# Kernel tuning notes

Measured on AMD Instinct MI355X. Metric: run time of the kernel, lower is better.

## Reference

```python
import jax, jax.numpy as jnp
import numpy as np

B, S, H = 2, 2048, 2048
N_HEADS = 16
HEAD_DIM = H // N_HEADS


def setup_inputs() -> dict:
    key = jax.random.key(0)
    ks = jax.random.split(key, 9)
    s = 1.0 / np.sqrt(H)
    inp = {
        "x": jax.random.normal(ks[0], (B, S, H), dtype=jnp.float32),
        "wq": jax.random.uniform(ks[1], (H, H), jnp.float32, -s, s),
        "bq": jnp.zeros((H,), jnp.float32),
        "wk": jax.random.uniform(ks[2], (H, H), jnp.float32, -s, s),
        "bk": jnp.zeros((H,), jnp.float32),
        "wv": jax.random.uniform(ks[3], (H, H), jnp.float32, -s, s),
        "bv": jnp.zeros((H,), jnp.float32),
        "wo": jax.random.uniform(ks[4], (H, H), jnp.float32, -s, s),
        "bo": jnp.zeros((H,), jnp.float32),
    }
    return inp


def reference(x, wq, bq, wk, bk, wv, bv, wo, bo):
    bsz, seq_len, hidden = x.shape
    scale = HEAD_DIM ** -0.5
    # projections -> [b, h, s, d]
    def proj(w, b):
        y = jnp.einsum("bsh,oh->bso", x, w) + b
        return y.reshape(bsz, seq_len, N_HEADS, HEAD_DIM).transpose(0, 2, 1, 3)
    q = proj(wq, bq)
    k = proj(wk, bk)
    v = proj(wv, bv)
    scores = jnp.einsum("bhqd,bhkd->bhqk", q, k) * scale
    causal = jnp.tril(jnp.ones((seq_len, seq_len), dtype=bool))
    scores = jnp.where(causal, scores, -jnp.inf)
    attn = jax.nn.softmax(scores, axis=-1)
    out = jnp.einsum("bhqk,bhkd->bhqd", attn, v)
    out = out.transpose(0, 2, 1, 3).reshape(bsz, seq_len, hidden)
    return jnp.einsum("bsh,oh->bso", out, wo) + bo
```

## Files before the change

### kernel.cpp

```cpp
#include <hip/hip_runtime.h>
#include <hip/hip_bf16.h>
#include <cstdint>
#include <cstddef>

#define BATCH 2
#define S_LEN 2048
#define HID   2048
#define NH    16
#define HD    128
#define ATT_TILES (32 * NH * BATCH)

typedef short bf16x8 __attribute__((ext_vector_type(8)));
typedef float f32x4  __attribute__((ext_vector_type(4)));

__device__ inline unsigned short f2bf(float f) {
    unsigned int u = __float_as_uint(f);
    unsigned int r = (u + 0x7fffu + ((u >> 16) & 1u)) >> 16;
    return (unsigned short)r;
}

__global__ __launch_bounds__(256) void conv_f32_bf16(const float* __restrict__ src,
                                                     unsigned short* __restrict__ dst,
                                                     long n) {
    long i = ((long)blockIdx.x * 256 + threadIdx.x) * 8;
    if (i >= n) return;
    const float4 a = *(const float4*)(src + i);
    const float4 b = *(const float4*)(src + i + 4);
    union { unsigned short u[8]; bf16x8 v; } o;
    o.u[0] = f2bf(a.x); o.u[1] = f2bf(a.y); o.u[2] = f2bf(a.z); o.u[3] = f2bf(a.w);
    o.u[4] = f2bf(b.x); o.u[5] = f2bf(b.y); o.u[6] = f2bf(b.z); o.u[7] = f2bf(b.w);
    *(bf16x8*)(dst + i) = o.v;
}

__global__ __launch_bounds__(256) void conv4_f32_bf16(const float* __restrict__ s0,
                                                      const float* __restrict__ s1,
                                                      const float* __restrict__ s2,
                                                      const float* __restrict__ s3,
                                                      unsigned short* __restrict__ d0,
                                                      unsigned short* __restrict__ d1,
                                                      unsigned short* __restrict__ d2,
                                                      unsigned short* __restrict__ d3,
                                                      long n) {
    const int z = blockIdx.y;
    const float* src = (z == 0) ? s0 : (z == 1) ? s1 : (z == 2) ? s2 : s3;
    unsigned short* dst = (z == 0) ? d0 : (z == 1) ? d1 : (z == 2) ? d2 : d3;
    long i = ((long)blockIdx.x * 256 + threadIdx.x) * 8;
    if (i >= n) return;
    const float4 a = *(const float4*)(src + i);
    const float4 b = *(const float4*)(src + i + 4);
    union { unsigned short u[8]; bf16x8 v; } o;
    o.u[0] = f2bf(a.x); o.u[1] = f2bf(a.y); o.u[2] = f2bf(a.z); o.u[3] = f2bf(a.w);
    o.u[4] = f2bf(b.x); o.u[5] = f2bf(b.y); o.u[6] = f2bf(b.z); o.u[7] = f2bf(b.w);
    *(bf16x8*)(dst + i) = o.v;
}

__global__ void zero_int(int* p) { *p = 0; }

__device__ __forceinline__ void gemm_core(const unsigned short* __restrict__ A,
                                          const unsigned short* __restrict__ Bw,
                                          const float* __restrict__ bias,
                                          void* __restrict__ Cout,
                                          int M, int N, int K, int mode,
                                          int m0, int n0,
                                          unsigned short* Sm) {
    unsigned short* As = Sm;
    unsigned short* Bs = Sm + 4096;
    const int tid = threadIdx.x;
    const int lane = tid & 63;
    const int wave = tid >> 6;
    const int g = lane >> 4, ln = lane & 15;
    const int wm = (wave & 1) * 64, wn = (wave >> 1) * 64;

    f32x4 acc[4][4];
#pragma unroll
    for (int i = 0; i < 4; ++i)
#pragma unroll
        for (int j = 0; j < 4; ++j) acc[i][j] = (f32x4){0.f, 0.f, 0.f, 0.f};

    const int srow = wave * 16 + (lane >> 2);
    const int scol = (((lane & 3) ^ ((lane >> 3) & 3)) * 8);
    const int rxor = (ln >> 1) & 3;

    for (int k0 = 0; k0 < K; k0 += 32) {
#pragma unroll
        for (int c = 0; c < 2; ++c) {
            const unsigned short* ga = A  + (size_t)(m0 + c * 64 + srow) * K + k0 + scol;
            const unsigned short* gb = Bw + (size_t)(n0 + c * 64 + srow) * K + k0 + scol;
            __builtin_amdgcn_global_load_lds(
                (const __attribute__((address_space(1))) void*)ga,
                (__attribute__((address_space(3))) void*)(As + c * 2048 + wave * 512),
                16, 0, 0);
            __builtin_amdgcn_global_load_lds(
                (const __attribute__((address_space(1))) void*)gb,
                (__attribute__((address_space(3))) void*)(Bs + c * 2048 + wave * 512),
                16, 0, 0);
        }
        __syncthreads();
        bf16x8 af[4], bfr[4];
#pragma unroll
        for (int t = 0; t < 4; ++t) {
            af[t]  = *(const bf16x8*)&As[(wm + t * 16 + ln) * 32 + (g ^ rxor) * 8];
            bfr[t] = *(const bf16x8*)&Bs[(wn + t * 16 + ln) * 32 + (g ^ rxor) * 8];
        }
#pragma unroll
        for (int mt = 0; mt < 4; ++mt)
#pragma unroll
            for (int nt = 0; nt < 4; ++nt)
                acc[mt][nt] = __builtin_amdgcn_mfma_f32_16x16x32_bf16(af[mt], bfr[nt], acc[mt][nt], 0, 0, 0);
        __syncthreads();
    }

    if (mode == 1) {
        const int b = m0 >> 11;
        const int sbase = m0 & 2047;
        const int h = n0 >> 7;
#pragma unroll
        for (int p2 = 0; p2 < 2; ++p2) {
            if ((wave >> 1) == p2) {
#pragma unroll
                for (int nt = 0; nt < 4; ++nt) {
                    const int dl = nt * 16 + ln;
                    const float bn = bias[n0 + p2 * 64 + dl];
#pragma unroll
                    for (int mt = 0; mt < 4; ++mt)
#pragma unroll
                        for (int r = 0; r < 4; ++r) {
                            const int sl = wm + mt * 16 + g * 4 + r;
                            const int psc = (sl >> 3) ^ (dl & 15);
                            Sm[dl * 128 + psc * 8 + (sl & 7)] = f2bf(acc[mt][nt][r] + bn);
                        }
                }
            }
            __syncthreads();
            const int dl = tid >> 2;
            const int dd = p2 * 64 + dl;
            unsigned short* dst = (unsigned short*)Cout +
                ((size_t)(b * NH + h) * HD + dd) * S_LEN + sbase;
#pragma unroll
            for (int j = 0; j < 4; ++j) {
                const int sc = (tid & 3) * 4 + j;
                const int psc = sc ^ (dl & 15);
                *(bf16x8*)(dst + sc * 8) = *(const bf16x8*)&Sm[dl * 128 + psc * 8];
            }
            __syncthreads();
        }
        return;
    }

#pragma unroll
    for (int mt = 0; mt < 4; ++mt)
#pragma unroll
        for (int nt = 0; nt < 4; ++nt) {
            const int n = n0 + wn + nt * 16 + ln;
            const float bn = bias[n];
#pragma unroll
            for (int r = 0; r < 4; ++r) {
                const int m = m0 + wm + mt * 16 + g * 4 + r;
                const float v = acc[mt][nt][r] + bn;
                if (mode == 2) {
                    ((float*)Cout)[(size_t)m * N + n] = v;
                } else {
                    const int b = m >> 11, s = m & 2047;
                    const int h = n >> 7, d = n & 127;
                    ((unsigned short*)Cout)[((((size_t)b * NH + h) * S_LEN + s) * HD + d)] = f2bf(v);
                }
            }
        }
}

__global__ __launch_bounds__(256) void gemm_qkv(const unsigned short* __restrict__ A,
                                                const unsigned short* __restrict__ w0,
                                                const unsigned short* __restrict__ w1,
                                                const unsigned short* __restrict__ w2,
                                                const float* __restrict__ b0,
                                                const float* __restrict__ b1,
                                                const float* __restrict__ b2,
                                                void* o0, void* o1, void* o2,
                                                int M, int N, int K) {
    __shared__ __align__(16) unsigned short Sm[8192];
    const int z = blockIdx.z;
    const unsigned short* Bw = (z == 0) ? w0 : (z == 1) ? w1 : w2;
    const float* bias = (z == 0) ? b0 : (z == 1) ? b1 : b2;
    void* Cout = (z == 0) ? o0 : (z == 1) ? o1 : o2;
    const int mode = (z == 2) ? 1 : 0;
    gemm_core(A, Bw, bias, Cout, M, N, K, mode,
              blockIdx.y * 128, blockIdx.x * 128, Sm);
}

__global__ __launch_bounds__(256) void gemm_bt(const unsigned short* __restrict__ A,
                                               const unsigned short* __restrict__ Bw,
                                               const float* __restrict__ bias,
                                               void* __restrict__ Cout,
                                               int M, int N, int K, int mode) {
    __shared__ __align__(16) unsigned short Sm[8192];
    gemm_core(A, Bw, bias, Cout, M, N, K, mode,
              blockIdx.y * 128, blockIdx.x * 128, Sm);
}

__global__ __launch_bounds__(256) void attn_kernel(const unsigned short* __restrict__ Q,
                                                   const unsigned short* __restrict__ Kk,
                                                   const unsigned short* __restrict__ Vt,
                                                   unsigned short* __restrict__ O,
                                                   int* __restrict__ ticket) {
    __shared__ __align__(16) unsigned short Ks[64 * 128];
    __shared__ __align__(16) unsigned short Vs[144 * 64];
    __shared__ __align__(16) unsigned short Pl[4][16 * 72];
    __shared__ int tsh;
    const int tid = threadIdx.x;
    const int lane = tid & 63;
    const int wave = tid >> 6;
    const int g = lane >> 4, ln = lane & 15;
    const float scale2 = 0.08838834764831845f * 1.4426950408889634f;

    for (int i = tid; i < 16 * 64; i += 256) Vs[128 * 64 + i] = 0x3F80;

    const int kcol = ((tid & 15) ^ ((tid >> 4) & 15)) * 8;
    const int vcol = ((tid & 7) ^ ((tid >> 3) & 7)) * 8;

    for (;;) {
        if (tid == 0) tsh = atomicAdd(ticket, 1);
        __syncthreads();
        const int t = tsh;
        if (t >= ATT_TILES) break;
        const int qt = 31 - (t >> 5);
        const int bh = t & 31;
        const int qbase = qt * 64 + wave * 16;

        const unsigned short* Qp = Q  + (size_t)bh * S_LEN * HD;
        const unsigned short* Kp = Kk + (size_t)bh * S_LEN * HD;
        const unsigned short* Vp = Vt + (size_t)bh * HD * S_LEN;

        bf16x8 aq[4];
#pragma unroll
        for (int dc = 0; dc < 4; ++dc)
            aq[dc] = *(const bf16x8*)&Qp[(size_t)(qbase + ln) * HD + dc * 32 + g * 8];

        f32x4 acc[9];
#pragma unroll
        for (int i = 0; i < 9; ++i) acc[i] = (f32x4){0.f, 0.f, 0.f, 0.f};

        for (int kt = 0; kt <= qt; ++kt) {
            const int kb = kt * 64;
#pragma unroll
            for (int i = 0; i < 4; ++i) {
                const unsigned short* gk = Kp + (size_t)(kb + i * 16 + (tid >> 4)) * HD + kcol;
                __builtin_amdgcn_global_load_lds(
                    (const __attribute__((address_space(1))) void*)gk,
                    (__attribute__((address_space(3))) void*)(Ks + i * 2048 + wave * 512),
                    16, 0, 0);
            }
#pragma unroll
            for (int i = 0; i < 4; ++i) {
                const unsigned short* gv = Vp + (size_t)(i * 32 + (tid >> 3)) * S_LEN + kb + vcol;
                __builtin_amdgcn_global_load_lds(
                    (const __attribute__((address_space(1))) void*)gv,
                    (__attribute__((address_space(3))) void*)(Vs + i * 2048 + wave * 512),
                    16, 0, 0);
            }
            __syncthreads();
            f32x4 sc[4];
#pragma unroll
            for (int nc = 0; nc < 4; ++nc) {
                sc[nc] = (f32x4){0.f, 0.f, 0.f, 0.f};
#pragma unroll
                for (int dc = 0; dc < 4; ++dc) {
                    bf16x8 bk = *(const bf16x8*)&Ks[(nc * 16 + ln) * 128 + ((dc * 4 + g) ^ ln) * 8];
                    sc[nc] = __builtin_amdgcn_mfma_f32_16x16x32_bf16(aq[dc], bk, sc[nc], 0, 0, 0);
                }
            }
            const bool diag = (kt == qt);
#pragma unroll
            for (int nc = 0; nc < 4; ++nc)
#pragma unroll
                for (int r = 0; r < 4; ++r) {
                    float pv = __builtin_amdgcn_exp2f(sc[nc][r] * scale2);
                    if (diag && (nc * 16 + ln > wave * 16 + g * 4 + r)) pv = 0.f;
                    Pl[wave][(g * 4 + r) * 72 + nc * 16 + ln] = f2bf(pv);
                }
#pragma unroll
            for (int kc = 0; kc < 2; ++kc) {
                bf16x8 ap = *(const bf16x8*)&Pl[wave][ln * 72 + kc * 32 + g * 8];
#pragma unroll
                for (int d2 = 0; d2 < 9; ++d2) {
                    bf16x8 bv = *(const bf16x8*)&Vs[(d2 * 16 + ln) * 64 + ((kc * 4 + g) ^ (ln & 7)) * 8];
                    acc[d2] = __builtin_amdgcn_mfma_f32_16x16x32_bf16(ap, bv, acc[d2], 0, 0, 0);
                }
            }
            __syncthreads();
        }
        const int b = bh >> 4, h = bh & 15;
        float inv[4];
#pragma unroll
        for (int r = 0; r < 4; ++r) inv[r] = 1.0f / acc[8][r];
#pragma unroll
        for (int d2 = 0; d2 < 8; ++d2)
#pragma unroll
            for (int r = 0; r < 4; ++r) {
                const int row = qbase + g * 4 + r;
                const int col = h * HD + d2 * 16 + ln;
                O[((size_t)b * S_LEN + row) * HID + col] = f2bf(acc[d2][r] * inv[r]);
            }
    }
}

extern "C" void kernel_launch(void* const* d_in, const int* in_sizes, int n_in,
                              void* d_out, int out_size, void* d_ws, size_t ws_size,
                              hipStream_t stream) {
    const float* x  = (const float*)d_in[0];
    const float* wq = (const float*)d_in[1];
    const float* bq = (const float*)d_in[2];
    const float* wk = (const float*)d_in[3];
    const float* bk = (const float*)d_in[4];
    const float* wv = (const float*)d_in[5];
    const float* bv = (const float*)d_in[6];
    const float* wo = (const float*)d_in[7];
    const float* bo = (const float*)d_in[8];
    float* out = (float*)d_out;

    const long nx = (long)BATCH * S_LEN * HID;
    const long nw = (long)HID * HID;

    char* p = (char*)d_ws;
    unsigned short* xb  = (unsigned short*)p; p += nx * 2;
    unsigned short* wqb = (unsigned short*)p; p += nw * 2;
    unsigned short* wkb = (unsigned short*)p; p += nw * 2;
    unsigned short* wvb = (unsigned short*)p; p += nw * 2;
    unsigned short* wob = (unsigned short*)p; p += nw * 2;
    unsigned short* Qb  = (unsigned short*)p; p += nx * 2;
    unsigned short* Kb  = (unsigned short*)p; p += nx * 2;
    unsigned short* Vtb = (unsigned short*)p; p += nx * 2;
    unsigned short* Ob  = (unsigned short*)p; p += nx * 2;
    int* ticket = (int*)p;

    conv_f32_bf16<<<(int)(nx / 8 / 256), 256, 0, stream>>>(x, xb, nx);
    dim3 cgrid((unsigned)(nw / 8 / 256), 4);
    conv4_f32_bf16<<<cgrid, 256, 0, stream>>>(wq, wk, wv, wo, wqb, wkb, wvb, wob, nw);
    zero_int<<<1, 1, 0, stream>>>(ticket);

    const int M = BATCH * S_LEN;
    dim3 qkvgrid(HID / 128, M / 128, 3);
    gemm_qkv<<<qkvgrid, 256, 0, stream>>>(xb, wqb, wkb, wvb, bq, bk, bv,
                                          Qb, Kb, Vtb, M, HID, HID);

    attn_kernel<<<768, 256, 0, stream>>>(Qb, Kb, Vtb, Ob, ticket);

    dim3 ggrid(HID / 128, M / 128);
    gemm_bt<<<ggrid, 256, 0, stream>>>(Ob, wob, bo, out, M, HID, HID, 2);
}
```

Before: 433.5 us.

## Use 128-row attention tiles with 8 waves and split-K output GEMM with atomics

```diff
diff --git a/kernel.cpp b/kernel.cpp
--- a/kernel.cpp
+++ b/kernel.cpp
@@ -8,7 +8,7 @@
 #define HID   2048
 #define NH    16
 #define HD    128
-#define ATT_TILES (32 * NH * BATCH)
+#define ATT_TILES2 (16 * NH * BATCH)
 
 typedef short bf16x8 __attribute__((ext_vector_type(8)));
 typedef float f32x4  __attribute__((ext_vector_type(4)));
@@ -56,12 +56,17 @@
 
 __global__ void zero_int(int* p) { *p = 0; }
 
+__global__ __launch_bounds__(256) void zero_f32(float4* __restrict__ p, long n4) {
+    long i = (long)blockIdx.x * 256 + threadIdx.x;
+    if (i < n4) p[i] = (float4){0.f, 0.f, 0.f, 0.f};
+}
+
 __device__ __forceinline__ void gemm_core(const unsigned short* __restrict__ A,
                                           const unsigned short* __restrict__ Bw,
                                           const float* __restrict__ bias,
                                           void* __restrict__ Cout,
                                           int M, int N, int K, int mode,
-                                          int m0, int n0,
+                                          int m0, int n0, int kbeg, int kend,
                                           unsigned short* Sm) {
     unsigned short* As = Sm;
     unsigned short* Bs = Sm + 4096;
@@ -81,7 +86,7 @@
     const int scol = (((lane & 3) ^ ((lane >> 3) & 3)) * 8);
     const int rxor = (ln >> 1) & 3;
 
-    for (int k0 = 0; k0 < K; k0 += 32) {
+    for (int k0 = kbeg; k0 < kend; k0 += 32) {
 #pragma unroll
         for (int c = 0; c < 2; ++c) {
             const unsigned short* ga = A  + (size_t)(m0 + c * 64 + srow) * K + k0 + scol;
@@ -152,13 +157,13 @@
 #pragma unroll
         for (int nt = 0; nt < 4; ++nt) {
             const int n = n0 + wn + nt * 16 + ln;
-            const float bn = bias[n];
+            const float bn = (mode != 3 || kbeg == 0) ? bias[n] : 0.f;
 #pragma unroll
             for (int r = 0; r < 4; ++r) {
                 const int m = m0 + wm + mt * 16 + g * 4 + r;
                 const float v = acc[mt][nt][r] + bn;
-                if (mode == 2) {
-                    ((float*)Cout)[(size_t)m * N + n] = v;
+                if (mode == 3) {
+                    atomicAdd(&((float*)Cout)[(size_t)m * N + n], v);
                 } else {
                     const int b = m >> 11, s = m & 2047;
                     const int h = n >> 7, d = n & 127;
@@ -184,27 +189,29 @@
     void* Cout = (z == 0) ? o0 : (z == 1) ? o1 : o2;
     const int mode = (z == 2) ? 1 : 0;
     gemm_core(A, Bw, bias, Cout, M, N, K, mode,
-              blockIdx.y * 128, blockIdx.x * 128, Sm);
-}
-
-__global__ __launch_bounds__(256) void gemm_bt(const unsigned short* __restrict__ A,
-                                               const unsigned short* __restrict__ Bw,
-                                               const float* __restrict__ bias,
-                                               void* __restrict__ Cout,
-                                               int M, int N, int K, int mode) {
+              blockIdx.y * 128, blockIdx.x * 128, 0, K, Sm);
+}
+
+__global__ __launch_bounds__(256) void gemm_out(const unsigned short* __restrict__ A,
+                                                const unsigned short* __restrict__ Bw,
+                                                const float* __restrict__ bias,
+                                                void* __restrict__ Cout,
+                                                int M, int N, int K) {
     __shared__ __align__(16) unsigned short Sm[8192];
-    gemm_core(A, Bw, bias, Cout, M, N, K, mode,
-              blockIdx.y * 128, blockIdx.x * 128, Sm);
-}
-
-__global__ __launch_bounds__(256) void attn_kernel(const unsigned short* __restrict__ Q,
+    const int kh = K / 2;
+    gemm_core(A, Bw, bias, Cout, M, N, K, 3,
+              blockIdx.y * 128, blockIdx.x * 128,
+              blockIdx.z * kh, blockIdx.z * kh + kh, Sm);
+}
+
+__global__ __launch_bounds__(512) void attn_kernel(const unsigned short* __restrict__ Q,
                                                    const unsigned short* __restrict__ Kk,
                                                    const unsigned short* __restrict__ Vt,
                                                    unsigned short* __restrict__ O,
                                                    int* __restrict__ ticket) {
     __shared__ __align__(16) unsigned short Ks[64 * 128];
     __shared__ __align__(16) unsigned short Vs[144 * 64];
-    __shared__ __align__(16) unsigned short Pl[4][16 * 72];
+    __shared__ __align__(16) unsigned short Pl[8][16 * 72];
     __shared__ int tsh;
     const int tid = threadIdx.x;
     const int lane = tid & 63;
@@ -212,7 +219,7 @@
     const int g = lane >> 4, ln = lane & 15;
     const float scale2 = 0.08838834764831845f * 1.4426950408889634f;
 
-    for (int i = tid; i < 16 * 64; i += 256) Vs[128 * 64 + i] = 0x3F80;
+    for (int i = tid; i < 16 * 64; i += 512) Vs[128 * 64 + i] = 0x3F80;
 
     const int kcol = ((tid & 15) ^ ((tid >> 4) & 15)) * 8;
     const int vcol = ((tid & 7) ^ ((tid >> 3) & 7)) * 8;
@@ -221,10 +228,10 @@
         if (tid == 0) tsh = atomicAdd(ticket, 1);
         __syncthreads();
         const int t = tsh;
-        if (t >= ATT_TILES) break;
-        const int qt = 31 - (t >> 5);
+        if (t >= ATT_TILES2) break;
+        const int qt = 15 - (t >> 5);
         const int bh = t & 31;
-        const int qbase = qt * 64 + wave * 16;
+        const int qbase = qt * 128 + wave * 16;
 
         const unsigned short* Qp = Q  + (size_t)bh * S_LEN * HD;
         const unsigned short* Kp = Kk + (size_t)bh * S_LEN * HD;
@@ -239,51 +246,56 @@
 #pragma unroll
         for (int i = 0; i < 9; ++i) acc[i] = (f32x4){0.f, 0.f, 0.f, 0.f};
 
-        for (int kt = 0; kt <= qt; ++kt) {
+        const int ktend = 2 * qt + 1;
+        const int myktmax = 2 * qt + (wave >> 2);
+        for (int kt = 0; kt <= ktend; ++kt) {
             const int kb = kt * 64;
 #pragma unroll
-            for (int i = 0; i < 4; ++i) {
-                const unsigned short* gk = Kp + (size_t)(kb + i * 16 + (tid >> 4)) * HD + kcol;
+            for (int i = 0; i < 2; ++i) {
+                const unsigned short* gk = Kp + (size_t)(kb + i * 32 + (tid >> 4)) * HD + kcol;
                 __builtin_amdgcn_global_load_lds(
                     (const __attribute__((address_space(1))) void*)gk,
-                    (__attribute__((address_space(3))) void*)(Ks + i * 2048 + wave * 512),
+                    (__attribute__((address_space(3))) void*)(Ks + i * 4096 + wave * 512),
                     16, 0, 0);
             }
 #pragma unroll
-            for (int i = 0; i < 4; ++i) {
-                const unsigned short* gv = Vp + (size_t)(i * 32 + (tid >> 3)) * S_LEN + kb + vcol;
+            for (int i = 0; i < 2; ++i) {
+                const unsigned short* gv = Vp + (size_t)(i * 64 + (tid >> 3)) * S_LEN + kb + vcol;
                 __builtin_amdgcn_global_load_lds(
                     (const __attribute__((address_space(1))) void*)gv,
-                    (__attribute__((address_space(3))) void*)(Vs + i * 2048 + wave * 512),
+                    (__attribute__((address_space(3))) void*)(Vs + i * 4096 + wave * 512),
                     16, 0, 0);
             }
             __syncthreads();
-            f32x4 sc[4];
-#pragma unroll
-            for (int nc = 0; nc < 4; ++nc) {
-                sc[nc] = (f32x4){0.f, 0.f, 0.f, 0.f};
-#pragma unroll
-                for (int dc = 0; dc < 4; ++dc) {
-                    bf16x8 bk = *(const bf16x8*)&Ks[(nc * 16 + ln) * 128 + ((dc * 4 + g) ^ ln) * 8];
-                    sc[nc] = __builtin_amdgcn_mfma_f32_16x16x32_bf16(aq[dc], bk, sc[nc], 0, 0, 0);
+            if (kt <= myktmax) {
+                f32x4 sc[4];
+#pragma unroll
+                for (int nc = 0; nc < 4; ++nc) {
+                    sc[nc] = (f32x4){0.f, 0.f, 0.f, 0.f};
+#pragma unroll
+                    for (int dc = 0; dc < 4; ++dc) {
+                        bf16x8 bk = *(const bf16x8*)&Ks[(nc * 16 + ln) * 128 + ((dc * 4 + g) ^ ln) * 8];
+                        sc[nc] = __builtin_amdgcn_mfma_f32_16x16x32_bf16(aq[dc], bk, sc[nc], 0, 0, 0);
+                    }
                 }
-            }
-            const bool diag = (kt == qt);
-#pragma unroll
-            for (int nc = 0; nc < 4; ++nc)
-#pragma unroll
-                for (int r = 0; r < 4; ++r) {
-                    float pv = __builtin_amdgcn_exp2f(sc[nc][r] * scale2);
-                    if (diag && (nc * 16 + ln > wave * 16 + g * 4 + r)) pv = 0.f;
-                    Pl[wave][(g * 4 + r) * 72 + nc * 16 + ln] = f2bf(pv);
-                }
-#pragma unroll
-            for (int kc = 0; kc < 2; ++kc) {
-                bf16x8 ap = *(const bf16x8*)&Pl[wave][ln * 72 + kc * 32 + g * 8];
-#pragma unroll
-                for (int d2 = 0; d2 < 9; ++d2) {
-                    bf16x8 bv = *(const bf16x8*)&Vs[(d2 * 16 + ln) * 64 + ((kc * 4 + g) ^ (ln & 7)) * 8];
-                    acc[d2] = __builtin_amdgcn_mfma_f32_16x16x32_bf16(ap, bv, acc[d2], 0, 0, 0);
+                const bool diag = (kt == myktmax);
+                const int lrow = (wave & 3) * 16;
+#pragma unroll
+                for (int nc = 0; nc < 4; ++nc)
+#pragma unroll
+                    for (int r = 0; r < 4; ++r) {
+                        float pv = __builtin_amdgcn_exp2f(sc[nc][r] * scale2);
+                        if (diag && (nc * 16 + ln > lrow + g * 4 + r)) pv = 0.f;
+                        Pl[wave][(g * 4 + r) * 72 + nc * 16 + ln] = f2bf(pv);
+                    }
+#pragma unroll
+                for (int kc = 0; kc < 2; ++kc) {
+                    bf16x8 ap = *(const bf16x8*)&Pl[wave][ln * 72 + kc * 32 + g * 8];
+#pragma unroll
+                    for (int d2 = 0; d2 < 9; ++d2) {
+                        bf16x8 bv = *(const bf16x8*)&Vs[(d2 * 16 + ln) * 64 + ((kc * 4 + g) ^ (ln & 7)) * 8];
+                        acc[d2] = __builtin_amdgcn_mfma_f32_16x16x32_bf16(ap, bv, acc[d2], 0, 0, 0);
+                    }
                 }
             }
             __syncthreads();
@@ -336,14 +348,15 @@
     dim3 cgrid((unsigned)(nw / 8 / 256), 4);
     conv4_f32_bf16<<<cgrid, 256, 0, stream>>>(wq, wk, wv, wo, wqb, wkb, wvb, wob, nw);
     zero_int<<<1, 1, 0, stream>>>(ticket);
+    zero_f32<<<(int)(nx / 4 / 256), 256, 0, stream>>>((float4*)out, nx / 4);
 
     const int M = BATCH * S_LEN;
     dim3 qkvgrid(HID / 128, M / 128, 3);
     gemm_qkv<<<qkvgrid, 256, 0, stream>>>(xb, wqb, wkb, wvb, bq, bk, bv,
                                           Qb, Kb, Vtb, M, HID, HID);
 
-    attn_kernel<<<768, 256, 0, stream>>>(Qb, Kb, Vtb, Ob, ticket);
-
-    dim3 ggrid(HID / 128, M / 128);
-    gemm_bt<<<ggrid, 256, 0, stream>>>(Ob, wob, bo, out, M, HID, HID, 2);
-}
+    attn_kernel<<<512, 512, 0, stream>>>(Qb, Kb, Vtb, Ob, ticket);
+
+    dim3 ogrid(HID / 128, M / 128, 2);
+    gemm_out<<<ogrid, 256, 0, stream>>>(Ob, wob, bo, out, M, HID, HID);
+}
```

Result: slower. 466.4 us (+7.6%).

## Fuse Q and K projections into one GEMM sharing the activation tile

Applied to the files above, without the earlier changes.

```diff
diff --git a/kernel.cpp b/kernel.cpp
--- a/kernel.cpp
+++ b/kernel.cpp
@@ -56,19 +56,108 @@
 
 __global__ void zero_int(int* p) { *p = 0; }
 
-__device__ __forceinline__ void gemm_core(const unsigned short* __restrict__ A,
-                                          const unsigned short* __restrict__ Bw,
-                                          const float* __restrict__ bias,
-                                          void* __restrict__ Cout,
-                                          int M, int N, int K, int mode,
-                                          int m0, int n0,
-                                          unsigned short* Sm) {
+__global__ __launch_bounds__(256) void gemm_qk(const unsigned short* __restrict__ A,
+                                               const unsigned short* __restrict__ wqb,
+                                               const unsigned short* __restrict__ wkb,
+                                               const float* __restrict__ bq,
+                                               const float* __restrict__ bk,
+                                               unsigned short* __restrict__ Qo,
+                                               unsigned short* __restrict__ Ko,
+                                               int M, int N, int K) {
+    __shared__ __align__(16) unsigned short As [128 * 32];
+    __shared__ __align__(16) unsigned short Bsq[128 * 32];
+    __shared__ __align__(16) unsigned short Bsk[128 * 32];
+    const int tid = threadIdx.x;
+    const int lane = tid & 63;
+    const int wave = tid >> 6;
+    const int g = lane >> 4, ln = lane & 15;
+    const int m0 = blockIdx.y * 128, n0 = blockIdx.x * 128;
+    const int wm = (wave & 1) * 64, wn = (wave >> 1) * 64;
+
+    f32x4 accq[4][4], acck[4][4];
+#pragma unroll
+    for (int i = 0; i < 4; ++i)
+#pragma unroll
+        for (int j = 0; j < 4; ++j) {
+            accq[i][j] = (f32x4){0.f, 0.f, 0.f, 0.f};
+            acck[i][j] = (f32x4){0.f, 0.f, 0.f, 0.f};
+        }
+
+    const int srow = wave * 16 + (lane >> 2);
+    const int scol = (((lane & 3) ^ ((lane >> 3) & 3)) * 8);
+    const int rxor = (ln >> 1) & 3;
+
+    for (int k0 = 0; k0 < K; k0 += 32) {
+#pragma unroll
+        for (int c = 0; c < 2; ++c) {
+            const size_t roff = (size_t)(c * 64 + srow) * K + k0 + scol;
+            __builtin_amdgcn_global_load_lds(
+                (const __attribute__((address_space(1))) void*)(A + (size_t)m0 * K + roff),
+                (__attribute__((address_space(3))) void*)(As + c * 2048 + wave * 512), 16, 0, 0);
+            __builtin_amdgcn_global_load_lds(
+                (const __attribute__((address_space(1))) void*)(wqb + (size_t)n0 * K + roff),
+                (__attribute__((address_space(3))) void*)(Bsq + c * 2048 + wave * 512), 16, 0, 0);
+            __builtin_amdgcn_global_load_lds(
+                (const __attribute__((address_space(1))) void*)(wkb + (size_t)n0 * K + roff),
+                (__attribute__((address_space(3))) void*)(Bsk + c * 2048 + wave * 512), 16, 0, 0);
+        }
+        __syncthreads();
+        bf16x8 af[4], bfr[4];
+#pragma unroll
+        for (int t = 0; t < 4; ++t)
+            af[t] = *(const bf16x8*)&As[(wm + t * 16 + ln) * 32 + (g ^ rxor) * 8];
+#pragma unroll
+        for (int t = 0; t < 4; ++t)
+            bfr[t] = *(const bf16x8*)&Bsq[(wn + t * 16 + ln) * 32 + (g ^ rxor) * 8];
+#pragma unroll
+        for (int mt = 0; mt < 4; ++mt)
+#pragma unroll
+            for (int nt = 0; nt < 4; ++nt)
+                accq[mt][nt] = __builtin_amdgcn_mfma_f32_16x16x32_bf16(af[mt], bfr[nt], accq[mt][nt], 0, 0, 0);
+#pragma unroll
+        for (int t = 0; t < 4; ++t)
+            bfr[t] = *(const bf16x8*)&Bsk[(wn + t * 16 + ln) * 32 + (g ^ rxor) * 8];
+#pragma unroll
+        for (int mt = 0; mt < 4; ++mt)
+#pragma unroll
+            for (int nt = 0; nt < 4; ++nt)
+                acck[mt][nt] = __builtin_amdgcn_mfma_f32_16x16x32_bf16(af[mt], bfr[nt], acck[mt][nt], 0, 0, 0);
+        __syncthreads();
+    }
+
+    const int bb = m0 >> 11;
+    const int sbase = m0 & 2047;
+    const int hh = n0 >> 7;
+#pragma unroll
+    for (int mt = 0; mt < 4; ++mt)
+#pragma unroll
+        for (int nt = 0; nt < 4; ++nt) {
+            const int n = wn + nt * 16 + ln;
+            const float bnq = bq[n0 + n];
+            const float bnk = bk[n0 + n];
+#pragma unroll
+            for (int r = 0; r < 4; ++r) {
+                const int s = sbase + wm + mt * 16 + g * 4 + r;
+                const size_t idx = (((size_t)(bb * NH + hh) * S_LEN + s) * HD + n);
+                Qo[idx] = f2bf(accq[mt][nt][r] + bnq);
+                Ko[idx] = f2bf(acck[mt][nt][r] + bnk);
+            }
+        }
+}
+
+__global__ __launch_bounds__(256) void gemm_v(const unsigned short* __restrict__ A,
+                                              const unsigned short* __restrict__ Bw,
+                                              const float* __restrict__ bias,
+                                              unsigned short* __restrict__ Vo,
+                                              int M, int N, int K) {
+    __shared__ __align__(16) unsigned short Sm[8192];
     unsigned short* As = Sm;
     unsigned short* Bs = Sm + 4096;
     const int tid = threadIdx.x;
     const int lane = tid & 63;
     const int wave = tid >> 6;
     const int g = lane >> 4, ln = lane & 15;
+    const int m0 = blockIdx.y * 128, n0 = blockIdx.x * 128;
     const int wm = (wave & 1) * 64, wn = (wave >> 1) * 64;
 
     f32x4 acc[4][4];
@@ -88,12 +177,10 @@
             const unsigned short* gb = Bw + (size_t)(n0 + c * 64 + srow) * K + k0 + scol;
             __builtin_amdgcn_global_load_lds(
                 (const __attribute__((address_space(1))) void*)ga,
-                (__attribute__((address_space(3))) void*)(As + c * 2048 + wave * 512),
-                16, 0, 0);
+                (__attribute__((address_space(3))) void*)(As + c * 2048 + wave * 512), 16, 0, 0);
             __builtin_amdgcn_global_load_lds(
                 (const __attribute__((address_space(1))) void*)gb,
-                (__attribute__((address_space(3))) void*)(Bs + c * 2048 + wave * 512),
-                16, 0, 0);
+                (__attribute__((address_space(3))) void*)(Bs + c * 2048 + wave * 512), 16, 0, 0);
         }
         __syncthreads();
         bf16x8 af[4], bfr[4];
@@ -110,41 +197,89 @@
         __syncthreads();
     }
 
-    if (mode == 1) {
-        const int b = m0 >> 11;
-        const int sbase = m0 & 2047;
-        const int h = n0 >> 7;
-#pragma unroll
-        for (int p2 = 0; p2 < 2; ++p2) {
-            if ((wave >> 1) == p2) {
-#pragma unroll
-                for (int nt = 0; nt < 4; ++nt) {
-                    const int dl = nt * 16 + ln;
-                    const float bn = bias[n0 + p2 * 64 + dl];
-#pragma unroll
-                    for (int mt = 0; mt < 4; ++mt)
-#pragma unroll
-                        for (int r = 0; r < 4; ++r) {
-                            const int sl = wm + mt * 16 + g * 4 + r;
-                            const int psc = (sl >> 3) ^ (dl & 15);
-                            Sm[dl * 128 + psc * 8 + (sl & 7)] = f2bf(acc[mt][nt][r] + bn);
-                        }
-                }
-            }
-            __syncthreads();
-            const int dl = tid >> 2;
-            const int dd = p2 * 64 + dl;
-            unsigned short* dst = (unsigned short*)Cout +
-                ((size_t)(b * NH + h) * HD + dd) * S_LEN + sbase;
-#pragma unroll
-            for (int j = 0; j < 4; ++j) {
-                const int sc = (tid & 3) * 4 + j;
-                const int psc = sc ^ (dl & 15);
-                *(bf16x8*)(dst + sc * 8) = *(const bf16x8*)&Sm[dl * 128 + psc * 8];
-            }
-            __syncthreads();
-        }
-        return;
+    const int b = m0 >> 11;
+    const int sbase = m0 & 2047;
+    const int h = n0 >> 7;
+#pragma unroll
+    for (int p2 = 0; p2 < 2; ++p2) {
+        if ((wave >> 1) == p2) {
+#pragma unroll
+            for (int nt = 0; nt < 4; ++nt) {
+                const int dl = nt * 16 + ln;
+                const float bn = bias[n0 + p2 * 64 + dl];
+#pragma unroll
+                for (int mt = 0; mt < 4; ++mt)
+#pragma unroll
+                    for (int r = 0; r < 4; ++r) {
+                        const int sl = wm + mt * 16 + g * 4 + r;
+                        const int psc = (sl >> 3) ^ (dl & 15);
+                        Sm[dl * 128 + psc * 8 + (sl & 7)] = f2bf(acc[mt][nt][r] + bn);
+                    }
+            }
+        }
+        __syncthreads();
+        const int dl = tid >> 2;
+        const int dd = p2 * 64 + dl;
+        unsigned short* dst = Vo + ((size_t)(b * NH + h) * HD + dd) * S_LEN + sbase;
+#pragma unroll
+        for (int j = 0; j < 4; ++j) {
+            const int sc = (tid & 3) * 4 + j;
+            const int psc = sc ^ (dl & 15);
+            *(bf16x8*)(dst + sc * 8) = *(const bf16x8*)&Sm[dl * 128 + psc * 8];
+        }
+        __syncthreads();
+    }
+}
+
+__global__ __launch_bounds__(256) void gemm_bt(const unsigned short* __restrict__ A,
+                                               const unsigned short* __restrict__ Bw,
+                                               const float* __restrict__ bias,
+                                               float* __restrict__ Cout,
+                                               int M, int N, int K) {
+    __shared__ __align__(16) unsigned short As[128 * 32];
+    __shared__ __align__(16) unsigned short Bs[128 * 32];
+    const int tid = threadIdx.x;
+    const int lane = tid & 63;
+    const int wave = tid >> 6;
+    const int g = lane >> 4, ln = lane & 15;
+    const int m0 = blockIdx.y * 128, n0 = blockIdx.x * 128;
+    const int wm = (wave & 1) * 64, wn = (wave >> 1) * 64;
+
+    f32x4 acc[4][4];
+#pragma unroll
+    for (int i = 0; i < 4; ++i)
+#pragma unroll
+        for (int j = 0; j < 4; ++j) acc[i][j] = (f32x4){0.f, 0.f, 0.f, 0.f};
+
+    const int srow = wave * 16 + (lane >> 2);
+    const int scol = (((lane & 3) ^ ((lane >> 3) & 3)) * 8);
+    const int rxor = (ln >> 1) & 3;
+
+    for (int k0 = 0; k0 < K; k0 += 32) {
+#pragma unroll
+        for (int c = 0; c < 2; ++c) {
+            const unsigned short* ga = A  + (size_t)(m0 + c * 64 + srow) * K + k0 + scol;
+            const unsigned short* gb = Bw + (size_t)(n0 + c * 64 + srow) * K + k0 + scol;
+            __builtin_amdgcn_global_load_lds(
+                (const __attribute__((address_space(1))) void*)ga,
+                (__attribute__((address_space(3))) void*)(As + c * 2048 + wave * 512), 16, 0, 0);
+            __builtin_amdgcn_global_load_lds(
+                (const __attribute__((address_space(1))) void*)gb,
+                (__attribute__((address_space(3))) void*)(Bs + c * 2048 + wave * 512), 16, 0, 0);
+        }
+        __syncthreads();
+        bf16x8 af[4], bfr[4];
+#pragma unroll
+        for (int t = 0; t < 4; ++t) {
+            af[t]  = *(const bf16x8*)&As[(wm + t * 16 + ln) * 32 + (g ^ rxor) * 8];
+            bfr[t] = *(const bf16x8*)&Bs[(wn + t * 16 + ln) * 32 + (g ^ rxor) * 8];
+        }
+#pragma unroll
+        for (int mt = 0; mt < 4; ++mt)
+#pragma unroll
+            for (int nt = 0; nt < 4; ++nt)
+                acc[mt][nt] = __builtin_amdgcn_mfma_f32_16x16x32_bf16(af[mt], bfr[nt], acc[mt][nt], 0, 0, 0);
+        __syncthreads();
     }
 
 #pragma unroll
@@ -156,45 +291,9 @@
 #pragma unroll
             for (int r = 0; r < 4; ++r) {
                 const int m = m0 + wm + mt * 16 + g * 4 + r;
-                const float v = acc[mt][nt][r] + bn;
-                if (mode == 2) {
-                    ((float*)Cout)[(size_t)m * N + n] = v;
-                } else {
-                    const int b = m >> 11, s = m & 2047;
-                    const int h = n >> 7, d = n & 127;
-                    ((unsigned short*)Cout)[((((size_t)b * NH + h) * S_LEN + s) * HD + d)] = f2bf(v);
-                }
-            }
-        }
-}
-
-__global__ __launch_bounds__(256) void gemm_qkv(const unsigned short* __restrict__ A,
-                                                const unsigned short* __restrict__ w0,
-                                                const unsigned short* __restrict__ w1,
-                                                const unsigned short* __restrict__ w2,
-                                                const float* __restrict__ b0,
-                                                const float* __restrict__ b1,
-                                                const float* __restrict__ b2,
-                                                void* o0, void* o1, void* o2,
-                                                int M, int N, int K) {
-    __shared__ __align__(16) unsigned short Sm[8192];
-    const int z = blockIdx.z;
-    const unsigned short* Bw = (z == 0) ? w0 : (z == 1) ? w1 : w2;
-    const float* bias = (z == 0) ? b0 : (z == 1) ? b1 : b2;
-    void* Cout = (z == 0) ? o0 : (z == 1) ? o1 : o2;
-    const int mode = (z == 2) ? 1 : 0;
-    gemm_core(A, Bw, bias, Cout, M, N, K, mode,
-              blockIdx.y * 128, blockIdx.x * 128, Sm);
-}
-
-__global__ __launch_bounds__(256) void gemm_bt(const unsigned short* __restrict__ A,
-                                               const unsigned short* __restrict__ Bw,
-                                               const float* __restrict__ bias,
-                                               void* __restrict__ Cout,
-                                               int M, int N, int K, int mode) {
-    __shared__ __align__(16) unsigned short Sm[8192];
-    gemm_core(A, Bw, bias, Cout, M, N, K, mode,
-              blockIdx.y * 128, blockIdx.x * 128, Sm);
+                Cout[(size_t)m * N + n] = acc[mt][nt][r] + bn;
+            }
+        }
 }
 
 __global__ __launch_bounds__(256) void attn_kernel(const unsigned short* __restrict__ Q,
@@ -246,16 +345,14 @@
                 const unsigned short* gk = Kp + (size_t)(kb + i * 16 + (tid >> 4)) * HD + kcol;
                 __builtin_amdgcn_global_load_lds(
                     (const __attribute__((address_space(1))) void*)gk,
-                    (__attribute__((address_space(3))) void*)(Ks + i * 2048 + wave * 512),
-                    16, 0, 0);
+                    (__attribute__((address_space(3))) void*)(Ks + i * 2048 + wave * 512), 16, 0, 0);
             }
 #pragma unroll
             for (int i = 0; i < 4; ++i) {
                 const unsigned short* gv = Vp + (size_t)(i * 32 + (tid >> 3)) * S_LEN + kb + vcol;
                 __builtin_amdgcn_global_load_lds(
                     (const __attribute__((address_space(1))) void*)gv,
-                    (__attribute__((address_space(3))) void*)(Vs + i * 2048 + wave * 512),
-                    16, 0, 0);
+                    (__attribute__((address_space(3))) void*)(Vs + i * 2048 + wave * 512), 16, 0, 0);
             }
             __syncthreads();
             f32x4 sc[4];
@@ -338,12 +435,12 @@
     zero_int<<<1, 1, 0, stream>>>(ticket);
 
     const int M = BATCH * S_LEN;
-    dim3 qkvgrid(HID / 128, M / 128, 3);
-    gemm_qkv<<<qkvgrid, 256, 0, stream>>>(xb, wqb, wkb, wvb, bq, bk, bv,
-                                          Qb, Kb, Vtb, M, HID, HID);
+    dim3 ggrid(HID / 128, M / 128);
+
+    gemm_qk<<<ggrid, 256, 0, stream>>>(xb, wqb, wkb, bq, bk, Qb, Kb, M, HID, HID);
+    gemm_v<<<ggrid, 256, 0, stream>>>(xb, wvb, bv, Vtb, M, HID, HID);
 
     attn_kernel<<<768, 256, 0, stream>>>(Qb, Kb, Vtb, Ob, ticket);
 
-    dim3 ggrid(HID / 128, M / 128);
-    gemm_bt<<<ggrid, 256, 0, stream>>>(Ob, wob, bo, out, M, HID, HID, 2);
-}
+    gemm_bt<<<ggrid, 256, 0, stream>>>(Ob, wob, bo, out, M, HID, HID);
+}
```

Result: slower. 474.7 us (+9.5%).
